# Performance work log

Hardware: AMD Instinct MI355X
Metric: run time of the kernel (lower is better)

## Reference

```python
import jax, jax.numpy as jnp
import numpy as np

EPS = 1e-7  # K.epsilon()
ROUTINGS = 3
NUM_CAPSULE = 8
FILTERS = 16


def squash(v, axis=-1):
    s2 = jnp.sum(jnp.square(v), axis=axis, keepdims=True)
    scale = s2 / (1.0 + s2) / jnp.sqrt(s2 + EPS)
    return scale * v


def _conv_per_caps(x, w):
    # x: [B,H,W,Cin], w: [k,k,Cin,Cout]
    return jax.lax.conv_general_dilated(
        x, w, window_strides=(1, 1), padding='SAME',
        dimension_numbers=('NHWC', 'HWIO', 'NHWC'))


def setup_inputs() -> dict:
    key = jax.random.key(0)
    k1, k2 = jax.random.split(key, 2)
    B, H, Wd, IN_CAPS, IN_F = 32, 32, 32, 8, 16
    input_tensor = jax.random.normal(k1, (B, H, Wd, IN_CAPS, IN_F), dtype=jnp.float32)
    # he_normal fan_in = k*k*Cin = 3*3*16 = 144
    W = jax.random.normal(k2, (IN_CAPS, 3, 3, IN_F, NUM_CAPSULE * FILTERS), dtype=jnp.float32) * np.sqrt(2.0 / 144.0)
    b = jnp.full((1, 1, NUM_CAPSULE, FILTERS), 0.1, dtype=jnp.float32)
    return {"input_tensor": input_tensor, "W": W, "b": b}


def reference(input_tensor, W, b):
    B, H, Wd, in_caps, in_f = input_tensor.shape
    # per-input-capsule conv: vmap over capsule axis of input and weight
    votes = jax.vmap(_conv_per_caps, in_axes=(3, 0), out_axes=1)(input_tensor, W)
    # [B, in_caps, H, W, num_cap*F] -> [B, in_caps, H, W, num_cap, F]
    votes = votes.reshape(B, in_caps, H, Wd, NUM_CAPSULE, FILTERS)

    # dynamic routing
    logits = jnp.zeros((B, in_caps, H, Wd, NUM_CAPSULE), dtype=votes.dtype)
    activation = None
    for i in range(ROUTINGS):
        route = jax.nn.softmax(logits, axis=-1)  # over output capsules
        # sum over input capsules of route-weighted votes, plus bias
        preactivate = jnp.einsum('bihwc,bihwcf->bhwcf', route, votes) + b
        activation = squash(preactivate, axis=-1)
        if i < ROUTINGS - 1:
            # scalar-product agreement
            logits = logits + jnp.einsum('bihwcf,bhwcf->bihwc', votes, activation)
    return activation.astype(jnp.float32)
```

## Files before the change

### kernel.cpp

```cpp
#include <hip/hip_runtime.h>
#include <math.h>


typedef _Float16 fp16x8 __attribute__((ext_vector_type(8)));
typedef float f32x4 __attribute__((ext_vector_type(4)));

#define EPS 1e-7f
constexpr int PSTRIDE = 136;
constexpr int PCOLS   = 18;
constexpr int LSTRIDE = 76;
constexpr int PXS     = 76;
constexpr int W_ELEMS = 40 * 8 * 64 * 8;

__device__ __forceinline__ float sumquad(float v) {
    v += __shfl_xor(v, 16);
    v += __shfl_xor(v, 32);
    return v;
}

__global__ __launch_bounds__(256)
void prep_weights(const float* __restrict__ wts,
                  _Float16* __restrict__ w16) {
    int n = blockIdx.x * 256 + threadIdx.x;
    if (n >= W_ELEMS) return;
    int j    = n & 7;
    int ln   = (n >> 3) & 63;
    int c0   = (n >> 9) & 7;
    int iq   = n >> 12;
    int i0   = iq / 5;
    int q0   = iq - i0 * 5;
    int k = q0 * 32 + (ln >> 4) * 8 + j;
    float w = 0.f;
    if (k < 144) w = wts[(i0 * 144 + k) * 128 + c0 * 16 + (ln & 15)];
    w16[n] = (_Float16)w;
}

__global__ __launch_bounds__(256, 4)
void capsule_mfma_kernel(const float* __restrict__ x,
                         const _Float16* __restrict__ w16,
                         const float* __restrict__ bias,
                         float* __restrict__ out)
{
    __shared__ _Float16 patch[3 * PCOLS * PSTRIDE];
    __shared__ float lg_arr[16 * LSTRIDE];
    __shared__ float r_arr[16 * PXS];

    const int tid  = threadIdx.x;
    const int lane = tid & 63;
    const int w    = tid >> 6;
    const int c0   = 2 * w;
    const int l15  = lane & 15;
    const int quad = lane >> 4;
    const int lane8 = lane * 8;

    const int bid  = blockIdx.x;
    const int half = bid & 1;
    const int h    = (bid >> 1) & 31;
    const int b    = bid >> 6;
    const int pxbase = half * 16;

    const float4* x4 = (const float4*)x;
    for (int idx = tid; idx < 3 * PCOLS * 32; idx += 256) {
        int ch4  = idx & 31;
        int slot = idx >> 5;
        int row  = slot / PCOLS;
        int colp = slot - row * PCOLS;
        int gh = h - 1 + row;
        int gw = pxbase + colp - 1;
        float4 v = {0.f, 0.f, 0.f, 0.f};
        if ((unsigned)gh < 32u && (unsigned)gw < 32u)
            v = x4[(((b * 32 + gh) * 32 + gw) << 5) + ch4];
        _Float16 ph[4];
        ph[0] = (_Float16)v.x; ph[1] = (_Float16)v.y;
        ph[2] = (_Float16)v.z; ph[3] = (_Float16)v.w;
        *(ushort4*)&patch[slot * PSTRIDE + ch4 * 4] = *(const ushort4*)ph;
    }
    __syncthreads();

    int a_off[5];
    #pragma unroll
    for (int q = 0; q < 5; ++q) {
        int tap = 2 * q + (quad >> 1);
        if (tap > 8) tap = 8;
        int dy = tap / 3, dx = tap - dy * 3;
        a_off[q] = (dy * PCOLS + l15 + dx) * PSTRIDE + (quad & 1) * 8;
    }

    f32x4 acc[2][8];
    #pragma unroll
    for (int cc = 0; cc < 2; ++cc)
        #pragma unroll
        for (int i = 0; i < 8; ++i) acc[cc][i] = (f32x4){0.f, 0.f, 0.f, 0.f};

    #pragma unroll
    for (int q = 0; q < 5; ++q) {
        #pragma unroll
        for (int i = 0; i < 8; ++i) {
            int woff = ((i * 5 + q) * 8 + c0) * 512 + lane8;
            fp16x8 a0 = *(const fp16x8*)(w16 + woff);
            fp16x8 a1 = *(const fp16x8*)(w16 + woff + 512);
            fp16x8 bb = *(const fp16x8*)(patch + a_off[q] + i * 16);
            acc[0][i] = __builtin_amdgcn_mfma_f32_16x16x32_f16(a0, bb, acc[0][i], 0, 0, 0);
            acc[1][i] = __builtin_amdgcn_mfma_f32_16x16x32_f16(a1, bb, acc[1][i], 0, 0, 0);
        }
    }

    float barr[2][4];
    #pragma unroll
    for (int cc = 0; cc < 2; ++cc) {
        float4 bb4 = *(const float4*)(bias + (c0 + cc) * 16 + quad * 4);
        barr[cc][0] = bb4.x; barr[cc][1] = bb4.y; barr[cc][2] = bb4.z; barr[cc][3] = bb4.w;
    }

    float actv[2][4];

    #pragma unroll
    for (int cc = 0; cc < 2; ++cc) {
        float pre[4];
        #pragma unroll
        for (int r = 0; r < 4; ++r) {
            float s = acc[cc][0][r] + acc[cc][1][r] + acc[cc][2][r] + acc[cc][3][r]
                    + acc[cc][4][r] + acc[cc][5][r] + acc[cc][6][r] + acc[cc][7][r];
            pre[r] = s * 0.125f + barr[cc][r];
        }
        float s2 = sumquad(pre[0]*pre[0] + pre[1]*pre[1] + pre[2]*pre[2] + pre[3]*pre[3]);
        float scale = s2 * __builtin_amdgcn_rsqf(s2 + EPS) * __builtin_amdgcn_rcpf(1.f + s2);
        #pragma unroll
        for (int r = 0; r < 4; ++r) actv[cc][r] = scale * pre[r];
    }
    #pragma unroll
    for (int cc = 0; cc < 2; ++cc)
        #pragma unroll
        for (int i = 0; i < 8; ++i) {
            float t = acc[cc][i][0]*actv[cc][0] + acc[cc][i][1]*actv[cc][1]
                    + acc[cc][i][2]*actv[cc][2] + acc[cc][i][3]*actv[cc][3];
            t = sumquad(t);
            if (quad == 0) lg_arr[l15 * LSTRIDE + i * 9 + (c0 + cc)] = t;
        }
    __syncthreads();
    if (tid < 128) {
        int p = tid >> 3, ii = tid & 7;
        const float* lrow = &lg_arr[p * LSTRIDE + ii * 9];
        float m = lrow[0];
        #pragma unroll
        for (int cc = 1; cc < 8; ++cc) m = fmaxf(m, lrow[cc]);
        float e[8]; float den = 0.f;
        #pragma unroll
        for (int cc = 0; cc < 8; ++cc) { e[cc] = __expf(lrow[cc] - m); den += e[cc]; }
        float rd = __builtin_amdgcn_rcpf(den);
        #pragma unroll
        for (int cc = 0; cc < 8; ++cc) r_arr[p * PXS + cc * 8 + ii] = e[cc] * rd;
    }
    __syncthreads();

    #pragma unroll
    for (int cc = 0; cc < 2; ++cc) {
        const float4* rp = (const float4*)&r_arr[l15 * PXS + (c0 + cc) * 8];
        float4 r0 = rp[0], r1 = rp[1];
        float pre[4];
        #pragma unroll
        for (int r = 0; r < 4; ++r) {
            float s;
            s  = r0.x * acc[cc][0][r]; s = fmaf(r0.y, acc[cc][1][r], s);
            s  = fmaf(r0.z, acc[cc][2][r], s); s = fmaf(r0.w, acc[cc][3][r], s);
            s  = fmaf(r1.x, acc[cc][4][r], s); s = fmaf(r1.y, acc[cc][5][r], s);
            s  = fmaf(r1.z, acc[cc][6][r], s); s = fmaf(r1.w, acc[cc][7][r], s);
            pre[r] = s + barr[cc][r];
        }
        float s2 = sumquad(pre[0]*pre[0] + pre[1]*pre[1] + pre[2]*pre[2] + pre[3]*pre[3]);
        float scale = s2 * __builtin_amdgcn_rsqf(s2 + EPS) * __builtin_amdgcn_rcpf(1.f + s2);
        #pragma unroll
        for (int r = 0; r < 4; ++r) actv[cc][r] = scale * pre[r];
    }
    #pragma unroll
    for (int cc = 0; cc < 2; ++cc)
        #pragma unroll
        for (int i = 0; i < 8; ++i) {
            float t = acc[cc][i][0]*actv[cc][0] + acc[cc][i][1]*actv[cc][1]
                    + acc[cc][i][2]*actv[cc][2] + acc[cc][i][3]*actv[cc][3];
            t = sumquad(t);
            if (quad == 0) lg_arr[l15 * LSTRIDE + i * 9 + (c0 + cc)] += t;
        }
    __syncthreads();
    if (tid < 128) {
        int p = tid >> 3, ii = tid & 7;
        const float* lrow = &lg_arr[p * LSTRIDE + ii * 9];
        float m = lrow[0];
        #pragma unroll
        for (int cc = 1; cc < 8; ++cc) m = fmaxf(m, lrow[cc]);
        float e[8]; float den = 0.f;
        #pragma unroll
        for (int cc = 0; cc < 8; ++cc) { e[cc] = __expf(lrow[cc] - m); den += e[cc]; }
        float rd = __builtin_amdgcn_rcpf(den);
        #pragma unroll
        for (int cc = 0; cc < 8; ++cc) r_arr[p * PXS + cc * 8 + ii] = e[cc] * rd;
    }
    __syncthreads();

    #pragma unroll
    for (int cc = 0; cc < 2; ++cc) {
        const float4* rp = (const float4*)&r_arr[l15 * PXS + (c0 + cc) * 8];
        float4 r0 = rp[0], r1 = rp[1];
        float pre[4];
        #pragma unroll
        for (int r = 0; r < 4; ++r) {
            float s;
            s  = r0.x * acc[cc][0][r]; s = fmaf(r0.y, acc[cc][1][r], s);
            s  = fmaf(r0.z, acc[cc][2][r], s); s = fmaf(r0.w, acc[cc][3][r], s);
            s  = fmaf(r1.x, acc[cc][4][r], s); s = fmaf(r1.y, acc[cc][5][r], s);
            s  = fmaf(r1.z, acc[cc][6][r], s); s = fmaf(r1.w, acc[cc][7][r], s);
            pre[r] = s + barr[cc][r];
        }
        float s2 = sumquad(pre[0]*pre[0] + pre[1]*pre[1] + pre[2]*pre[2] + pre[3]*pre[3]);
        float scale = s2 * __builtin_amdgcn_rsqf(s2 + EPS) * __builtin_amdgcn_rcpf(1.f + s2);
        float4 o4 = { scale*pre[0], scale*pre[1], scale*pre[2], scale*pre[3] };
        int px = pxbase + l15;
        *(float4*)(out + (((b * 32 + h) * 32 + px) << 7) + (c0 + cc) * 16 + quad * 4) = o4;
    }
}

extern "C" void kernel_launch(void* const* d_in, const int* in_sizes, int n_in,
                              void* d_out, int out_size, void* d_ws, size_t ws_size,
                              hipStream_t stream) {
    const float* x    = (const float*)d_in[0];
    const float* wts  = (const float*)d_in[1];
    const float* bias = (const float*)d_in[2];
    float* out        = (float*)d_out;
    _Float16* w16     = (_Float16*)d_ws;

    prep_weights<<<dim3(640), dim3(256), 0, stream>>>(wts, w16);
    capsule_mfma_kernel<<<dim3(2048), dim3(256), 0, stream>>>(x, w16, bias, out);
}
```

Before: 107.7 us.

## Enlarge block tile to two output rows by full width with 1024 threads

Each block now covers two output rows across all 32 columns using 16 waves instead of 16 pixels with 4 waves, and loads a 4x34 input patch. This lowers the halo overhead of patch loading, since 4 input rows are shared by 2 output rows instead of 3 rows per output row. It also cuts the grid to 512 blocks. The cost is a much larger LDS footprint, block-wide barriers across 1024 threads, and fewer blocks to spread over the CUs, which could reduce latency hiding.

```diff
diff --git a/kernel.cpp b/kernel.cpp
--- a/kernel.cpp
+++ b/kernel.cpp
@@ -7,7 +7,8 @@
 
 #define EPS 1e-7f
 constexpr int PSTRIDE = 136;
-constexpr int PCOLS   = 18;
+constexpr int PCOLS   = 34;
+constexpr int PROWS   = 4;
 constexpr int LSTRIDE = 76;
 constexpr int PXS     = 76;
 constexpr int W_ELEMS = 40 * 8 * 64 * 8;
@@ -35,38 +36,39 @@
     w16[n] = (_Float16)w;
 }
 
-__global__ __launch_bounds__(256, 4)
+__global__ __launch_bounds__(1024, 4)
 void capsule_mfma_kernel(const float* __restrict__ x,
                          const _Float16* __restrict__ w16,
                          const float* __restrict__ bias,
                          float* __restrict__ out)
 {
-    __shared__ _Float16 patch[3 * PCOLS * PSTRIDE];
-    __shared__ float lg_arr[16 * LSTRIDE];
-    __shared__ float r_arr[16 * PXS];
+    __shared__ _Float16 patch[PROWS * PCOLS * PSTRIDE];
+    __shared__ float lg_arr[64 * LSTRIDE];
+    __shared__ float r_arr[64 * PXS];
 
     const int tid  = threadIdx.x;
     const int lane = tid & 63;
     const int w    = tid >> 6;
-    const int c0   = 2 * w;
+    const int cp   = w & 3;
+    const int g    = (w >> 2) & 1;
+    const int mt   = w >> 3;
+    const int c0   = 2 * cp;
     const int l15  = lane & 15;
     const int quad = lane >> 4;
     const int lane8 = lane * 8;
 
-    const int bid  = blockIdx.x;
-    const int half = bid & 1;
-    const int h    = (bid >> 1) & 31;
-    const int b    = bid >> 6;
-    const int pxbase = half * 16;
+    const int bid = blockIdx.x;
+    const int h2 = bid & 15, b = bid >> 4;
+    const int h = h2 << 1;
 
     const float4* x4 = (const float4*)x;
-    for (int idx = tid; idx < 3 * PCOLS * 32; idx += 256) {
+    for (int idx = tid; idx < PROWS * PCOLS * 32; idx += 1024) {
         int ch4  = idx & 31;
         int slot = idx >> 5;
         int row  = slot / PCOLS;
         int colp = slot - row * PCOLS;
         int gh = h - 1 + row;
-        int gw = pxbase + colp - 1;
+        int gw = colp - 1;
         float4 v = {0.f, 0.f, 0.f, 0.f};
         if ((unsigned)gh < 32u && (unsigned)gw < 32u)
             v = x4[(((b * 32 + gh) * 32 + gw) << 5) + ch4];
@@ -83,7 +85,7 @@
         int tap = 2 * q + (quad >> 1);
         if (tap > 8) tap = 8;
         int dy = tap / 3, dx = tap - dy * 3;
-        a_off[q] = (dy * PCOLS + l15 + dx) * PSTRIDE + (quad & 1) * 8;
+        a_off[q] = ((g + dy) * PCOLS + mt * 16 + l15 + dx) * PSTRIDE + (quad & 1) * 8;
     }
 
     f32x4 acc[2][8];
@@ -105,6 +107,8 @@
         }
     }
 
+    const int slot = g * 32 + mt * 16 + l15;
+
     float barr[2][4];
     #pragma unroll
     for (int cc = 0; cc < 2; ++cc) {
@@ -135,10 +139,10 @@
             float t = acc[cc][i][0]*actv[cc][0] + acc[cc][i][1]*actv[cc][1]
                     + acc[cc][i][2]*actv[cc][2] + acc[cc][i][3]*actv[cc][3];
             t = sumquad(t);
-            if (quad == 0) lg_arr[l15 * LSTRIDE + i * 9 + (c0 + cc)] = t;
-        }
-    __syncthreads();
-    if (tid < 128) {
+            if (quad == 0) lg_arr[slot * LSTRIDE + i * 9 + (c0 + cc)] = t;
+        }
+    __syncthreads();
+    if (tid < 512) {
         int p = tid >> 3, ii = tid & 7;
         const float* lrow = &lg_arr[p * LSTRIDE + ii * 9];
         float m = lrow[0];
@@ -155,7 +159,7 @@
 
     #pragma unroll
     for (int cc = 0; cc < 2; ++cc) {
-        const float4* rp = (const float4*)&r_arr[l15 * PXS + (c0 + cc) * 8];
+        const float4* rp = (const float4*)&r_arr[slot * PXS + (c0 + cc) * 8];
         float4 r0 = rp[0], r1 = rp[1];
         float pre[4];
         #pragma unroll
@@ -179,10 +183,10 @@
             float t = acc[cc][i][0]*actv[cc][0] + acc[cc][i][1]*actv[cc][1]
                     + acc[cc][i][2]*actv[cc][2] + acc[cc][i][3]*actv[cc][3];
             t = sumquad(t);
-            if (quad == 0) lg_arr[l15 * LSTRIDE + i * 9 + (c0 + cc)] += t;
-        }
-    __syncthreads();
-    if (tid < 128) {
+            if (quad == 0) lg_arr[slot * LSTRIDE + i * 9 + (c0 + cc)] += t;
+        }
+    __syncthreads();
+    if (tid < 512) {
         int p = tid >> 3, ii = tid & 7;
         const float* lrow = &lg_arr[p * LSTRIDE + ii * 9];
         float m = lrow[0];
@@ -199,7 +203,7 @@
 
     #pragma unroll
     for (int cc = 0; cc < 2; ++cc) {
-        const float4* rp = (const float4*)&r_arr[l15 * PXS + (c0 + cc) * 8];
+        const float4* rp = (const float4*)&r_arr[slot * PXS + (c0 + cc) * 8];
         float4 r0 = rp[0], r1 = rp[1];
         float pre[4];
         #pragma unroll
@@ -214,8 +218,9 @@
         float s2 = sumquad(pre[0]*pre[0] + pre[1]*pre[1] + pre[2]*pre[2] + pre[3]*pre[3]);
         float scale = s2 * __builtin_amdgcn_rsqf(s2 + EPS) * __builtin_amdgcn_rcpf(1.f + s2);
         float4 o4 = { scale*pre[0], scale*pre[1], scale*pre[2], scale*pre[3] };
-        int px = pxbase + l15;
-        *(float4*)(out + (((b * 32 + h) * 32 + px) << 7) + (c0 + cc) * 16 + quad * 4) = o4;
+        int gh = h + g;
+        int px = mt * 16 + l15;
+        *(float4*)(out + (((b * 32 + gh) * 32 + px) << 7) + (c0 + cc) * 16 + quad * 4) = o4;
     }
 }
 
@@ -229,5 +234,5 @@
     _Float16* w16     = (_Float16*)d_ws;
 
     prep_weights<<<dim3(640), dim3(256), 0, stream>>>(wts, w16);
-    capsule_mfma_kernel<<<dim3(2048), dim3(256), 0, stream>>>(x, w16, bias, out);
-}
+    capsule_mfma_kernel<<<dim3(512), dim3(1024), 0, stream>>>(x, w16, bias, out);
+}
```

Result: slower. 114.7 us (+6.5%).
